# Kernel tuning notes

Hardware: AMD Instinct MI355X
Metric: run time of the kernel (lower is better)

Reference implementation:

```python
import jax, jax.numpy as jnp
import numpy as np

DIM = 1024
HEADS = 8
SCALE = 64 ** (-0.5)  # module uses dimHead=64 even though per-head c = DIM//HEADS = 128
LN_EPS = 1e-3  # keras LayerNormalization default


def _layernorm(t, g, b):
    mu = jnp.mean(t, axis=-1, keepdims=True)
    var = jnp.mean(jnp.square(t - mu), axis=-1, keepdims=True)
    return (t - mu) * jax.lax.rsqrt(var + LN_EPS) * g + b


def setup_inputs() -> dict:
    key = jax.random.key(0)
    ks = jax.random.split(key, 4)
    B, N, D = 4, 2048, DIM
    x = jax.random.normal(ks[0], (B, N, D), dtype=jnp.float32)
    w3 = jax.random.normal(ks[1], (D, 3 * D), dtype=jnp.float32) * (1.0 / np.sqrt(D))
    w1 = jax.random.normal(ks[2], (D, 4 * D), dtype=jnp.float32) * (1.0 / np.sqrt(D))
    w2 = jax.random.normal(ks[3], (4 * D, D), dtype=jnp.float32) * (1.0 / np.sqrt(4 * D))
    return {
        "x": x,
        "ln_g": jnp.ones((D,), jnp.float32),
        "ln_b": jnp.zeros((D,), jnp.float32),
        "w3": w3,
        "b3": jnp.zeros((3 * D,), jnp.float32),
        "w1": w1,
        "b1": jnp.zeros((4 * D,), jnp.float32),
        "w2": w2,
        "b2": jnp.zeros((D,), jnp.float32),
    }


def reference(x, ln_g, ln_b, w3, b3, w1, b1, w2, b2):
    B, N, D = x.shape
    H = HEADS
    C = D // H  # per-head channel dim

    # --- attention branch ---
    y = _layernorm(x, ln_g, ln_b)
    qkv = jax.nn.relu(y @ w3 + b3)  # [B, N, 3D] (note: relu on QKV, as in source)
    # einops 'b n (c h i) -> i b h n c' with i=3: last axis factors as (C, H, 3)
    qkv = qkv.reshape(B, N, C, H, 3)
    qkv = jnp.transpose(qkv, (4, 0, 3, 1, 2))  # [3, B, H, N, C]
    q, k, v = qkv[0], qkv[1], qkv[2]
    scores = jnp.einsum("bhqc,bhkc->bhqk", q, k) * SCALE
    attn = jax.nn.softmax(scores, axis=-1)
    o = jnp.einsum("bhqk,bhkc->bhqc", attn, v)  # [B, H, N, C]
    # 'b h n c -> b n (h c)'
    o = jnp.transpose(o, (0, 2, 1, 3)).reshape(B, N, H * C)
    y = o + x

    # --- MLP branch (shared layernorm params; dropout is identity at inference) ---
    y1 = _layernorm(y, ln_g, ln_b)
    mlp = jax.nn.relu(y1 @ w1 + b1) @ w2 + b2
    return mlp + y
```

## Files before the change

### kernel.cpp

```cpp
#include <hip/hip_runtime.h>
#include <hip/hip_bf16.h>
#include <cstdint>

typedef __attribute__((ext_vector_type(8))) __bf16 bf16x8;
typedef __attribute__((ext_vector_type(4))) float f32x4;
typedef unsigned short u16;

#define DEV static __device__ __forceinline__

constexpr float ATT_SCALE = 0.125f;
constexpr float LN_EPS = 1e-3f;

DEV void gload16(const void* g, void* l) {
  __builtin_amdgcn_global_load_lds((__attribute__((address_space(1))) void*)(g),
                                   (__attribute__((address_space(3))) void*)(l),
                                   16, 0, 0);
}

DEV u16 f2b(float f) { __hip_bfloat16 h = __float2bfloat16(f); return __builtin_bit_cast(u16, h); }

template<int PERM>
__global__ __launch_bounds__(256)
void k_transpose(const float* __restrict__ in, __hip_bfloat16* __restrict__ out,
                 int R, int C) {
  __shared__ float t[64][65];
  int d0 = blockIdx.x * 64, k0 = blockIdx.y * 64;
  int tid = threadIdx.x;
  int c64 = tid & 63, r4 = tid >> 6;
#pragma unroll
  for (int i = 0; i < 16; i++) {
    int kr = i * 4 + r4;
    t[c64][kr] = in[(size_t)(k0 + kr) * C + d0 + c64];
  }
  __syncthreads();
#pragma unroll
  for (int i = 0; i < 16; i++) {
    int dr = i * 4 + r4;
    int d = d0 + dr;
    int jp = PERM ? ((d % 3) * 1024 + ((d / 3) & 7) * 128 + (d / 24)) : d;
    out[(size_t)jp * R + k0 + c64] = __float2bfloat16(t[dr][c64]);
  }
}

__global__ __launch_bounds__(256)
void k_ln(const float* __restrict__ in, const float* __restrict__ g,
          const float* __restrict__ b, __hip_bfloat16* __restrict__ out) {
  int row = blockIdx.x, tid = threadIdx.x;
  const float4* in4 = (const float4*)(in + (size_t)row * 1024);
  float4 v = in4[tid];
  float s = v.x + v.y + v.z + v.w;
  float ss = v.x * v.x + v.y * v.y + v.z * v.z + v.w * v.w;
#pragma unroll
  for (int off = 32; off; off >>= 1) { s += __shfl_down(s, off); ss += __shfl_down(ss, off); }
  __shared__ float red[8];
  int w = tid >> 6, lane = tid & 63;
  if (lane == 0) { red[w] = s; red[4 + w] = ss; }
  __syncthreads();
  if (tid == 0) {
    float S = red[0] + red[1] + red[2] + red[3];
    float SS = red[4] + red[5] + red[6] + red[7];
    float mu = S * (1.f / 1024.f);
    float var = SS * (1.f / 1024.f) - mu * mu;
    red[0] = mu; red[1] = rsqrtf(var + LN_EPS);
  }
  __syncthreads();
  float mu = red[0], rs = red[1];
  int c = tid * 4;
  ushort4 o;
  o.x = f2b((v.x - mu) * rs * g[c + 0] + b[c + 0]);
  o.y = f2b((v.y - mu) * rs * g[c + 1] + b[c + 1]);
  o.z = f2b((v.z - mu) * rs * g[c + 2] + b[c + 2]);
  o.w = f2b((v.w - mu) * rs * g[c + 3] + b[c + 3]);
  ((ushort4*)((u16*)out + (size_t)row * 1024))[tid] = o;
}

template<int MODE>
__global__ __launch_bounds__(256, 2)
void k_gemm(const __hip_bfloat16* __restrict__ A,
            const __hip_bfloat16* __restrict__ Bt,
            const float* __restrict__ bias,
            const float* __restrict__ resid,
            float* __restrict__ outF,
            __hip_bfloat16* __restrict__ outQ,
            __hip_bfloat16* __restrict__ outK,
            __hip_bfloat16* __restrict__ outV,
            int K, int Nout) {
  __shared__ alignas(16) __hip_bfloat16 Asm[128 * 32];
  __shared__ alignas(16) __hip_bfloat16 Bsm[128 * 32];
  int tid = threadIdx.x, w = tid >> 6, lane = tid & 63;
  int wr = w >> 1, wc = w & 1;
  int lr = lane >> 4, lc = lane & 15;
  int m0 = blockIdx.y * 128, n0 = blockIdx.x * 128;
  f32x4 acc[4][4] = {};
  const __hip_bfloat16* aG = A + (size_t)(m0 + (tid >> 2)) * K + (tid & 3) * 8;
  const __hip_bfloat16* bG = Bt + (size_t)(n0 + (tid >> 2)) * K + (tid & 3) * 8;
  char* aB = (char*)Asm + w * 1024;
  char* bB = (char*)Bsm + w * 1024;
  for (int k0 = 0; k0 < K; k0 += 32) {
    gload16(aG + k0, aB);
    gload16(aG + (size_t)64 * K + k0, aB + 4096);
    gload16(bG + k0, bB);
    gload16(bG + (size_t)64 * K + k0, bB + 4096);
    __syncthreads();
    bf16x8 af[4], bfr[4];
#pragma unroll
    for (int mi = 0; mi < 4; mi++)
      af[mi] = *(const bf16x8*)(Asm + (wr * 64 + mi * 16 + lc) * 32 + lr * 8);
#pragma unroll
    for (int ni = 0; ni < 4; ni++)
      bfr[ni] = *(const bf16x8*)(Bsm + (wc * 64 + ni * 16 + lc) * 32 + lr * 8);
#pragma unroll
    for (int mi = 0; mi < 4; mi++)
#pragma unroll
      for (int ni = 0; ni < 4; ni++)
        acc[mi][ni] = __builtin_amdgcn_mfma_f32_16x16x32_bf16(af[mi], bfr[ni], acc[mi][ni], 0, 0, 0);
    __syncthreads();
  }
#pragma unroll
  for (int mi = 0; mi < 4; mi++) {
#pragma unroll
    for (int ni = 0; ni < 4; ni++) {
      int jp = n0 + wc * 64 + ni * 16 + lc;
#pragma unroll
      for (int r = 0; r < 4; r++) {
        int m = m0 + wr * 64 + mi * 16 + lr * 4 + r;
        float v = acc[mi][ni][r];
        if (MODE == 0) {
          int i = jp >> 10, h = (jp >> 7) & 7, c = jp & 127;
          v += bias[c * 24 + h * 3 + i];
          v = fmaxf(v, 0.f);
          __hip_bfloat16 bv = __float2bfloat16(v);
          int b_ = m >> 11, n = m & 2047;
          size_t bh = (size_t)(b_ * 8 + h);
          if (i == 0)      outQ[(bh * 2048 + n) * 128 + c] = bv;
          else if (i == 1) outK[(bh * 2048 + n) * 128 + c] = bv;
          else             outV[(bh * 128 + c) * 2048 + n] = bv;
        } else if (MODE == 1) {
          v += bias[jp];
          v = fmaxf(v, 0.f);
          outQ[(size_t)m * Nout + jp] = __float2bfloat16(v);
        } else {
          v += bias[jp] + resid[(size_t)m * Nout + jp];
          outF[(size_t)m * Nout + jp] = v;
        }
      }
    }
  }
}

__global__ __launch_bounds__(256, 3)
void k_attn(const __hip_bfloat16* __restrict__ qb,
            const __hip_bfloat16* __restrict__ kb,
            const __hip_bfloat16* __restrict__ vtb,
            const float* __restrict__ x,
            float* __restrict__ y) {
  __shared__ alignas(16) __hip_bfloat16 Kl[64 * 128];
  __shared__ alignas(16) __hip_bfloat16 Vl[128 * 64];
  __shared__ alignas(16) __hip_bfloat16 Pl[4 * 16 * 72];
  int tid = threadIdx.x, w = tid >> 6, lane = tid & 63;
  int lr = lane >> 4, lc = lane & 15;
  int sxz = (lc & 7) << 3;
  int qt = blockIdx.x, bh = blockIdx.y;
  int b_ = bh >> 3, h = bh & 7;
  int q0 = qt * 64;
  size_t bhN = (size_t)bh * 2048;

  bf16x8 qf[4];
#pragma unroll
  for (int ks = 0; ks < 4; ks++)
    qf[ks] = *(const bf16x8*)(qb + (bhN + q0 + w * 16 + lc) * 128 + ks * 32 + lr * 8);

  f32x4 oacc[8] = {};
  float mrun[4], lrun[4];
#pragma unroll
  for (int r = 0; r < 4; r++) { mrun[r] = -1e30f; lrun[r] = 0.f; }

  int krow = tid >> 4;
  int kcol = ((tid & 15) * 8) ^ ((krow & 7) << 3);
  const __hip_bfloat16* kG = kb + (bhN + krow) * 128 + kcol;
  int vrow = tid >> 3;
  int vcol = ((tid & 7) * 8) ^ ((vrow & 7) << 3);
  const __hip_bfloat16* vG = vtb + ((size_t)bh * 128 + vrow) * 2048 + vcol;
  char* kB = (char*)Kl + w * 1024;
  char* vB = (char*)Vl + w * 1024;

  for (int kv0 = 0; kv0 < 2048; kv0 += 64) {
#pragma unroll
    for (int p = 0; p < 4; p++)
      gload16(kG + (size_t)(kv0 + p * 16) * 128, kB + p * 4096);
#pragma unroll
    for (int p = 0; p < 4; p++)
      gload16(vG + kv0 + (size_t)p * 32 * 2048, vB + p * 4096);
    __syncthreads();

    f32x4 sf[4] = {};
#pragma unroll
    for (int ks = 0; ks < 4; ks++) {
      bf16x8 kfr[4];
#pragma unroll
      for (int ni = 0; ni < 4; ni++)
        kfr[ni] = *(const bf16x8*)(Kl + (ni * 16 + lc) * 128 + ((ks * 32 + lr * 8) ^ sxz));
#pragma unroll
      for (int ni = 0; ni < 4; ni++)
        sf[ni] = __builtin_amdgcn_mfma_f32_16x16x32_bf16(qf[ks], kfr[ni], sf[ni], 0, 0, 0);
    }

#pragma unroll
    for (int r = 0; r < 4; r++) {
      float tmax = fmaxf(fmaxf(sf[0][r], sf[1][r]), fmaxf(sf[2][r], sf[3][r]));
#pragma unroll
      for (int off = 1; off < 16; off <<= 1) tmax = fmaxf(tmax, __shfl_xor(tmax, off, 16));
      tmax *= ATT_SCALE;
      float mnew = fmaxf(mrun[r], tmax);
      float alpha = __expf(mrun[r] - mnew);
      mrun[r] = mnew;
      float rs = 0.f;
#pragma unroll
      for (int ni = 0; ni < 4; ni++) {
        float p = __expf(sf[ni][r] * ATT_SCALE - mnew);
        sf[ni][r] = p;
        rs += p;
      }
#pragma unroll
      for (int off = 1; off < 16; off <<= 1) rs += __shfl_xor(rs, off, 16);
      lrun[r] = lrun[r] * alpha + rs;
#pragma unroll
      for (int nc = 0; nc < 8; nc++) oacc[nc][r] *= alpha;
    }

#pragma unroll
    for (int ni = 0; ni < 4; ni++)
#pragma unroll
      for (int r = 0; r < 4; r++)
        Pl[w * 1152 + (lr * 4 + r) * 72 + ni * 16 + lc] = __float2bfloat16(sf[ni][r]);
    asm volatile("s_waitcnt lgkmcnt(0)" ::: "memory");

#pragma unroll
    for (int ks2 = 0; ks2 < 2; ks2++) {
      bf16x8 pa = *(const bf16x8*)(Pl + w * 1152 + lc * 72 + ks2 * 32 + lr * 8);
#pragma unroll
      for (int nc = 0; nc < 8; nc++) {
        bf16x8 vf = *(const bf16x8*)(Vl + (nc * 16 + lc) * 64 + ((ks2 * 32 + lr * 8) ^ sxz));
        oacc[nc] = __builtin_amdgcn_mfma_f32_16x16x32_bf16(pa, vf, oacc[nc], 0, 0, 0);
      }
    }
    __syncthreads();
  }

#pragma unroll
  for (int r = 0; r < 4; r++) {
    int n = q0 + w * 16 + lr * 4 + r;
    float inv = 1.f / lrun[r];
    size_t base = ((size_t)(b_ * 2048 + n)) * 1024 + h * 128;
#pragma unroll
    for (int nc = 0; nc < 8; nc++) {
      int c = nc * 16 + lc;
      y[base + c] = oacc[nc][r] * inv + x[base + c];
    }
  }
}

extern "C" void kernel_launch(void* const* d_in, const int* in_sizes, int n_in,
                              void* d_out, int out_size, void* d_ws, size_t ws_size,
                              hipStream_t stream) {
  const float* x   = (const float*)d_in[0];
  const float* lng = (const float*)d_in[1];
  const float* lnb = (const float*)d_in[2];
  const float* w3  = (const float*)d_in[3];
  const float* b3  = (const float*)d_in[4];
  const float* w1  = (const float*)d_in[5];
  const float* b1  = (const float*)d_in[6];
  const float* w2  = (const float*)d_in[7];
  const float* b2  = (const float*)d_in[8];
  float* out = (float*)d_out;

  constexpr size_t M = 8192;
  __hip_bfloat16* w3t  = (__hip_bfloat16*)d_ws;
  __hip_bfloat16* w1t  = w3t + (size_t)3072 * 1024;
  __hip_bfloat16* w2t  = w1t + (size_t)4096 * 1024;
  __hip_bfloat16* xln  = w2t + (size_t)4096 * 1024;
  __hip_bfloat16* qb   = xln + M * 1024;
  __hip_bfloat16* kbuf = qb + M * 1024;
  __hip_bfloat16* vtb  = kbuf + M * 1024;
  __hip_bfloat16* hmid = qb;

  k_transpose<1><<<dim3(48, 16), 256, 0, stream>>>(w3, w3t, 1024, 3072);
  k_transpose<0><<<dim3(64, 16), 256, 0, stream>>>(w1, w1t, 1024, 4096);
  k_transpose<0><<<dim3(16, 64), 256, 0, stream>>>(w2, w2t, 4096, 1024);
  k_ln<<<dim3(M), 256, 0, stream>>>(x, lng, lnb, xln);
  k_gemm<0><<<dim3(24, 64), 256, 0, stream>>>(xln, w3t, b3, nullptr, nullptr,
                                              qb, kbuf, vtb, 1024, 3072);
  k_attn<<<dim3(32, 32), 256, 0, stream>>>(qb, kbuf, vtb, x, out);
  k_ln<<<dim3(M), 256, 0, stream>>>(out, lng, lnb, xln);
  k_gemm<1><<<dim3(32, 64), 256, 0, stream>>>(xln, w1t, b1, nullptr, nullptr,
                                              hmid, nullptr, nullptr, 1024, 4096);
  k_gemm<2><<<dim3(8, 64), 256, 0, stream>>>(hmid, w2t, b2, out, out,
                                             nullptr, nullptr, nullptr, 4096, 1024);
}
```

Baseline: 569.4 us.

## Add triple-buffered 256-row GEMM for QKV/FC1 and double-buffer attention K/V

```diff
diff --git a/kernel.cpp b/kernel.cpp
--- a/kernel.cpp
+++ b/kernel.cpp
@@ -74,16 +74,118 @@
   ((ushort4*)((u16*)out + (size_t)row * 1024))[tid] = o;
 }
 
-template<int MODE>
+template<int NI, int MODE>
+__global__ __launch_bounds__(512, NI == 2 ? 4 : 2)
+void k_gemm2(const __hip_bfloat16* __restrict__ A,
+             const __hip_bfloat16* __restrict__ Bt,
+             const float* __restrict__ bias,
+             __hip_bfloat16* __restrict__ outQ,
+             __hip_bfloat16* __restrict__ outK,
+             __hip_bfloat16* __restrict__ outV,
+             int K, int Nout) {
+  constexpr int BN = NI * 64;
+  constexpr int ASZ = 256 * 32;
+  constexpr int BSZ = BN * 32;
+  constexpr int SLOT = ASZ + BSZ;
+  __shared__ alignas(16) __hip_bfloat16 lds[3 * SLOT];
+  int tid = threadIdx.x, wid = tid >> 6, lane = tid & 63;
+  int wr = wid >> 2, wc = wid & 3, lr = lane >> 4, lc = lane & 15;
+  int nwg = gridDim.x;
+  int wg = ((int)blockIdx.x & 7) * (nwg >> 3) + ((int)blockIdx.x >> 3);
+  int mtile = wg & 31, ntile = wg >> 5;
+  int m0 = mtile * 256, n0 = ntile * BN;
+  int NT = K >> 5;
+
+  int sw = ((tid >> 3) & 3) << 3;
+  const __hip_bfloat16* aS = A + (size_t)(m0 + (tid >> 2)) * K + (((tid & 3) * 8) ^ sw);
+  const __hip_bfloat16* bS = Bt + (size_t)(n0 + (tid >> 2)) * K + (((tid & 3) * 8) ^ sw);
+  const size_t K128 = (size_t)128 * K;
+
+  f32x4 acc[8][NI] = {};
+
+  auto STAGE = [&](int t, int slot) {
+    char* s = (char*)(lds + slot * SLOT);
+    const __hip_bfloat16* ap = aS + t * 32;
+    gload16(ap, s + tid * 16);
+    gload16(ap + K128, s + tid * 16 + 8192);
+    const __hip_bfloat16* bp = bS + t * 32;
+    gload16(bp, s + tid * 16 + 16384);
+    if constexpr (NI == 4) gload16(bp + K128, s + tid * 16 + 24576);
+  };
+
+  STAGE(0, 0); STAGE(1, 1);
+  if constexpr (NI == 2) asm volatile("s_waitcnt vmcnt(3)" ::: "memory");
+  else                   asm volatile("s_waitcnt vmcnt(4)" ::: "memory");
+  __builtin_amdgcn_s_barrier();
+  asm volatile("" ::: "memory");
+
+  int axor = ((lc >> 1) & 3) << 3;
+  int s_cur = 0;
+  for (int t = 0; t < NT; ++t) {
+    if (t + 2 < NT) { int s2 = s_cur + 2; if (s2 >= 3) s2 -= 3; STAGE(t + 2, s2); }
+    const __hip_bfloat16* As = lds + s_cur * SLOT;
+    const __hip_bfloat16* Bs = As + ASZ;
+    bf16x8 af[8], bfr[NI];
+#pragma unroll
+    for (int mi = 0; mi < 8; mi++)
+      af[mi] = *(const bf16x8*)(As + (wr * 128 + mi * 16 + lc) * 32 + ((lr * 8) ^ axor));
+#pragma unroll
+    for (int ni = 0; ni < NI; ni++)
+      bfr[ni] = *(const bf16x8*)(Bs + (wc * (BN / 4) + ni * 16 + lc) * 32 + ((lr * 8) ^ axor));
+    __builtin_amdgcn_s_setprio(1);
+#pragma unroll
+    for (int mi = 0; mi < 8; mi++)
+#pragma unroll
+      for (int ni = 0; ni < NI; ni++)
+        acc[mi][ni] = __builtin_amdgcn_mfma_f32_16x16x32_bf16(af[mi], bfr[ni], acc[mi][ni], 0, 0, 0);
+    __builtin_amdgcn_s_setprio(0);
+    if (t + 2 < NT) {
+      if constexpr (NI == 2) asm volatile("s_waitcnt vmcnt(3)" ::: "memory");
+      else                   asm volatile("s_waitcnt vmcnt(4)" ::: "memory");
+    } else {
+      asm volatile("s_waitcnt vmcnt(0)" ::: "memory");
+    }
+    asm volatile("" ::: "memory");
+    __builtin_amdgcn_s_barrier();
+    asm volatile("" ::: "memory");
+    s_cur = s_cur + 1; if (s_cur >= 3) s_cur = 0;
+  }
+
+#pragma unroll
+  for (int mi = 0; mi < 8; mi++) {
+#pragma unroll
+    for (int ni = 0; ni < NI; ni++) {
+      int jp = n0 + wc * (BN / 4) + ni * 16 + lc;
+#pragma unroll
+      for (int r = 0; r < 4; r++) {
+        int m = m0 + wr * 128 + mi * 16 + lr * 4 + r;
+        float v = acc[mi][ni][r];
+        if (MODE == 0) {
+          int i = jp >> 10, h = (jp >> 7) & 7, c = jp & 127;
+          v += bias[c * 24 + h * 3 + i];
+          v = fmaxf(v, 0.f);
+          __hip_bfloat16 bv = __float2bfloat16(v);
+          int b_ = m >> 11, n = m & 2047;
+          size_t bh = (size_t)(b_ * 8 + h);
+          if (i == 0)      outQ[(bh * 2048 + n) * 128 + c] = bv;
+          else if (i == 1) outK[(bh * 2048 + n) * 128 + c] = bv;
+          else             outV[(bh * 128 + c) * 2048 + n] = bv;
+        } else {
+          v += bias[jp];
+          v = fmaxf(v, 0.f);
+          outQ[(size_t)m * Nout + jp] = __float2bfloat16(v);
+        }
+      }
+    }
+  }
+}
+
 __global__ __launch_bounds__(256, 2)
 void k_gemm(const __hip_bfloat16* __restrict__ A,
             const __hip_bfloat16* __restrict__ Bt,
             const float* __restrict__ bias,
             const float* __restrict__ resid,
             float* __restrict__ outF,
-            __hip_bfloat16* __restrict__ outQ,
-            __hip_bfloat16* __restrict__ outK,
-            __hip_bfloat16* __restrict__ outV,
             int K, int Nout) {
   __shared__ alignas(16) __hip_bfloat16 Asm[128 * 32];
   __shared__ alignas(16) __hip_bfloat16 Bsm[128 * 32];
@@ -124,38 +226,21 @@
 #pragma unroll
       for (int r = 0; r < 4; r++) {
         int m = m0 + wr * 64 + mi * 16 + lr * 4 + r;
-        float v = acc[mi][ni][r];
-        if (MODE == 0) {
-          int i = jp >> 10, h = (jp >> 7) & 7, c = jp & 127;
-          v += bias[c * 24 + h * 3 + i];
-          v = fmaxf(v, 0.f);
-          __hip_bfloat16 bv = __float2bfloat16(v);
-          int b_ = m >> 11, n = m & 2047;
-          size_t bh = (size_t)(b_ * 8 + h);
-          if (i == 0)      outQ[(bh * 2048 + n) * 128 + c] = bv;
-          else if (i == 1) outK[(bh * 2048 + n) * 128 + c] = bv;
-          else             outV[(bh * 128 + c) * 2048 + n] = bv;
-        } else if (MODE == 1) {
-          v += bias[jp];
-          v = fmaxf(v, 0.f);
-          outQ[(size_t)m * Nout + jp] = __float2bfloat16(v);
-        } else {
-          v += bias[jp] + resid[(size_t)m * Nout + jp];
-          outF[(size_t)m * Nout + jp] = v;
-        }
+        float v = acc[mi][ni][r] + bias[jp] + resid[(size_t)m * Nout + jp];
+        outF[(size_t)m * Nout + jp] = v;
       }
     }
   }
 }
 
-__global__ __launch_bounds__(256, 3)
+__global__ __launch_bounds__(256, 2)
 void k_attn(const __hip_bfloat16* __restrict__ qb,
             const __hip_bfloat16* __restrict__ kb,
             const __hip_bfloat16* __restrict__ vtb,
             const float* __restrict__ x,
             float* __restrict__ y) {
-  __shared__ alignas(16) __hip_bfloat16 Kl[64 * 128];
-  __shared__ alignas(16) __hip_bfloat16 Vl[128 * 64];
+  __shared__ alignas(16) __hip_bfloat16 Kl[2][64 * 128];
+  __shared__ alignas(16) __hip_bfloat16 Vl[2][128 * 64];
   __shared__ alignas(16) __hip_bfloat16 Pl[4 * 16 * 72];
   int tid = threadIdx.x, w = tid >> 6, lane = tid & 63;
   int lr = lane >> 4, lc = lane & 15;
@@ -181,29 +266,40 @@
   int vrow = tid >> 3;
   int vcol = ((tid & 7) * 8) ^ ((vrow & 7) << 3);
   const __hip_bfloat16* vG = vtb + ((size_t)bh * 128 + vrow) * 2048 + vcol;
-  char* kB = (char*)Kl + w * 1024;
-  char* vB = (char*)Vl + w * 1024;
-
-  for (int kv0 = 0; kv0 < 2048; kv0 += 64) {
+
+  auto STAGEKV = [&](int kv0, int buf) {
+    char* kB = (char*)(&Kl[buf][0]) + w * 1024;
+    char* vB = (char*)(&Vl[buf][0]) + w * 1024;
 #pragma unroll
     for (int p = 0; p < 4; p++)
       gload16(kG + (size_t)(kv0 + p * 16) * 128, kB + p * 4096);
 #pragma unroll
     for (int p = 0; p < 4; p++)
       gload16(vG + kv0 + (size_t)p * 32 * 2048, vB + p * 4096);
-    __syncthreads();
+  };
+
+  STAGEKV(0, 0);
+  __syncthreads();
+
+  for (int it = 0; it < 32; ++it) {
+    int buf = it & 1;
+    if (it < 31) STAGEKV((it + 1) * 64, buf ^ 1);
+    const __hip_bfloat16* Kb = &Kl[buf][0];
+    const __hip_bfloat16* Vb = &Vl[buf][0];
 
     f32x4 sf[4] = {};
+    __builtin_amdgcn_s_setprio(1);
 #pragma unroll
     for (int ks = 0; ks < 4; ks++) {
       bf16x8 kfr[4];
 #pragma unroll
       for (int ni = 0; ni < 4; ni++)
-        kfr[ni] = *(const bf16x8*)(Kl + (ni * 16 + lc) * 128 + ((ks * 32 + lr * 8) ^ sxz));
+        kfr[ni] = *(const bf16x8*)(Kb + (ni * 16 + lc) * 128 + ((ks * 32 + lr * 8) ^ sxz));
 #pragma unroll
       for (int ni = 0; ni < 4; ni++)
         sf[ni] = __builtin_amdgcn_mfma_f32_16x16x32_bf16(qf[ks], kfr[ni], sf[ni], 0, 0, 0);
     }
+    __builtin_amdgcn_s_setprio(0);
 
 #pragma unroll
     for (int r = 0; r < 4; r++) {
@@ -235,15 +331,17 @@
         Pl[w * 1152 + (lr * 4 + r) * 72 + ni * 16 + lc] = __float2bfloat16(sf[ni][r]);
     asm volatile("s_waitcnt lgkmcnt(0)" ::: "memory");
 
+    __builtin_amdgcn_s_setprio(1);
 #pragma unroll
     for (int ks2 = 0; ks2 < 2; ks2++) {
       bf16x8 pa = *(const bf16x8*)(Pl + w * 1152 + lc * 72 + ks2 * 32 + lr * 8);
 #pragma unroll
       for (int nc = 0; nc < 8; nc++) {
-        bf16x8 vf = *(const bf16x8*)(Vl + (nc * 16 + lc) * 64 + ((ks2 * 32 + lr * 8) ^ sxz));
+        bf16x8 vf = *(const bf16x8*)(Vb + (nc * 16 + lc) * 64 + ((ks2 * 32 + lr * 8) ^ sxz));
         oacc[nc] = __builtin_amdgcn_mfma_f32_16x16x32_bf16(pa, vf, oacc[nc], 0, 0, 0);
       }
     }
+    __builtin_amdgcn_s_setprio(0);
     __syncthreads();
   }
 
@@ -288,12 +386,9 @@
   k_transpose<0><<<dim3(64, 16), 256, 0, stream>>>(w1, w1t, 1024, 4096);
   k_transpose<0><<<dim3(16, 64), 256, 0, stream>>>(w2, w2t, 4096, 1024);
   k_ln<<<dim3(M), 256, 0, stream>>>(x, lng, lnb, xln);
-  k_gemm<0><<<dim3(24, 64), 256, 0, stream>>>(xln, w3t, b3, nullptr, nullptr,
-                                              qb, kbuf, vtb, 1024, 3072);
+  k_gemm2<2, 0><<<dim3(768), 512, 0, stream>>>(xln, w3t, b3, qb, kbuf, vtb, 1024, 3072);
   k_attn<<<dim3(32, 32), 256, 0, stream>>>(qb, kbuf, vtb, x, out);
   k_ln<<<dim3(M), 256, 0, stream>>>(out, lng, lnb, xln);
-  k_gemm<1><<<dim3(32, 64), 256, 0, stream>>>(xln, w1t, b1, nullptr, nullptr,
-                                              hmid, nullptr, nullptr, 1024, 4096);
-  k_gemm<2><<<dim3(8, 64), 256, 0, stream>>>(hmid, w2t, b2, out, out,
-                                             nullptr, nullptr, nullptr, 4096, 1024);
-}
+  k_gemm2<4, 1><<<dim3(512), 512, 0, stream>>>(xln, w1t, b1, hmid, nullptr, nullptr, 1024, 4096);
+  k_gemm<<<dim3(8, 64), 256, 0, stream>>>(hmid, w2t, b2, out, out, 4096, 1024);
+}
```

Measured after the change: 603.3 us. +6.0%, slower.

## Double-buffer K tiles in attention with 512-thread blocks and lazy rescale

Applied to the files above, without the earlier changes.

```diff
diff --git a/kernel.cpp b/kernel.cpp
--- a/kernel.cpp
+++ b/kernel.cpp
@@ -148,21 +148,21 @@
   }
 }
 
-__global__ __launch_bounds__(256, 3)
+__global__ __launch_bounds__(512, 4)
 void k_attn(const __hip_bfloat16* __restrict__ qb,
             const __hip_bfloat16* __restrict__ kb,
             const __hip_bfloat16* __restrict__ vtb,
             const float* __restrict__ x,
             float* __restrict__ y) {
-  __shared__ alignas(16) __hip_bfloat16 Kl[64 * 128];
+  __shared__ alignas(16) __hip_bfloat16 Kl[2][64 * 128];
   __shared__ alignas(16) __hip_bfloat16 Vl[128 * 64];
-  __shared__ alignas(16) __hip_bfloat16 Pl[4 * 16 * 72];
+  __shared__ alignas(16) __hip_bfloat16 Pl[8 * 16 * 72];
   int tid = threadIdx.x, w = tid >> 6, lane = tid & 63;
   int lr = lane >> 4, lc = lane & 15;
   int sxz = (lc & 7) << 3;
   int qt = blockIdx.x, bh = blockIdx.y;
   int b_ = bh >> 3, h = bh & 7;
-  int q0 = qt * 64;
+  int q0 = qt * 128;
   size_t bhN = (size_t)bh * 2048;
 
   bf16x8 qf[4];
@@ -181,51 +181,79 @@
   int vrow = tid >> 3;
   int vcol = ((tid & 7) * 8) ^ ((vrow & 7) << 3);
   const __hip_bfloat16* vG = vtb + ((size_t)bh * 128 + vrow) * 2048 + vcol;
-  char* kB = (char*)Kl + w * 1024;
-  char* vB = (char*)Vl + w * 1024;
-
-  for (int kv0 = 0; kv0 < 2048; kv0 += 64) {
-#pragma unroll
-    for (int p = 0; p < 4; p++)
-      gload16(kG + (size_t)(kv0 + p * 16) * 128, kB + p * 4096);
-#pragma unroll
-    for (int p = 0; p < 4; p++)
-      gload16(vG + kv0 + (size_t)p * 32 * 2048, vB + p * 4096);
-    __syncthreads();
+
+  auto STAGE_K = [&](int kv0, int buf) {
+    char* kB = (char*)(&Kl[buf][0]) + w * 1024;
+#pragma unroll
+    for (int p = 0; p < 2; p++)
+      gload16(kG + (size_t)(kv0 + p * 32) * 128, kB + p * 8192);
+  };
+  auto STAGE_V = [&](int kv0) {
+    char* vB = (char*)(&Vl[0]) + w * 1024;
+#pragma unroll
+    for (int p = 0; p < 2; p++)
+      gload16(vG + kv0 + (size_t)p * 64 * 2048, vB + p * 8192);
+  };
+
+  STAGE_V(0);
+  STAGE_K(0, 0);
+  asm volatile("s_waitcnt vmcnt(0)" ::: "memory");
+  __syncthreads();
+
+  for (int it = 0; it < 32; ++it) {
+    int buf = it & 1;
+    if (it > 0) STAGE_V(it * 64);
+    if (it < 31) STAGE_K((it + 1) * 64, buf ^ 1);
+    const __hip_bfloat16* Kb = &Kl[buf][0];
 
     f32x4 sf[4] = {};
+    __builtin_amdgcn_s_setprio(1);
 #pragma unroll
     for (int ks = 0; ks < 4; ks++) {
       bf16x8 kfr[4];
 #pragma unroll
       for (int ni = 0; ni < 4; ni++)
-        kfr[ni] = *(const bf16x8*)(Kl + (ni * 16 + lc) * 128 + ((ks * 32 + lr * 8) ^ sxz));
+        kfr[ni] = *(const bf16x8*)(Kb + (ni * 16 + lc) * 128 + ((ks * 32 + lr * 8) ^ sxz));
 #pragma unroll
       for (int ni = 0; ni < 4; ni++)
         sf[ni] = __builtin_amdgcn_mfma_f32_16x16x32_bf16(qf[ks], kfr[ni], sf[ni], 0, 0, 0);
     }
-
+    __builtin_amdgcn_s_setprio(0);
+
+    float tmax[4];
+    bool need = false;
 #pragma unroll
     for (int r = 0; r < 4; r++) {
-      float tmax = fmaxf(fmaxf(sf[0][r], sf[1][r]), fmaxf(sf[2][r], sf[3][r]));
-#pragma unroll
-      for (int off = 1; off < 16; off <<= 1) tmax = fmaxf(tmax, __shfl_xor(tmax, off, 16));
-      tmax *= ATT_SCALE;
-      float mnew = fmaxf(mrun[r], tmax);
-      float alpha = __expf(mrun[r] - mnew);
-      mrun[r] = mnew;
+      float tm = fmaxf(fmaxf(sf[0][r], sf[1][r]), fmaxf(sf[2][r], sf[3][r]));
+#pragma unroll
+      for (int off = 1; off < 16; off <<= 1) tm = fmaxf(tm, __shfl_xor(tm, off, 16));
+      tm *= ATT_SCALE;
+      tmax[r] = tm;
+      need = need || (tm > mrun[r] + 8.f);
+    }
+    if (__any(need)) {
+#pragma unroll
+      for (int r = 0; r < 4; r++) {
+        float mnew = fmaxf(mrun[r], tmax[r]);
+        float alpha = __expf(mrun[r] - mnew);
+        mrun[r] = mnew;
+        lrun[r] *= alpha;
+#pragma unroll
+        for (int nc = 0; nc < 8; nc++) oacc[nc][r] *= alpha;
+      }
+    }
+#pragma unroll
+    for (int r = 0; r < 4; r++) {
       float rs = 0.f;
 #pragma unroll
       for (int ni = 0; ni < 4; ni++) {
-        float p = __expf(sf[ni][r] * ATT_SCALE - mnew);
+        float p = __expf(sf[ni][r] * ATT_SCALE - mrun[r]);
         sf[ni][r] = p;
         rs += p;
       }
 #pragma unroll
       for (int off = 1; off < 16; off <<= 1) rs += __shfl_xor(rs, off, 16);
-      lrun[r] = lrun[r] * alpha + rs;
-#pragma unroll
-      for (int nc = 0; nc < 8; nc++) oacc[nc][r] *= alpha;
+      lrun[r] += rs;
     }
 
 #pragma unroll
@@ -233,8 +261,12 @@
 #pragma unroll
       for (int r = 0; r < 4; r++)
         Pl[w * 1152 + (lr * 4 + r) * 72 + ni * 16 + lc] = __float2bfloat16(sf[ni][r]);
-    asm volatile("s_waitcnt lgkmcnt(0)" ::: "memory");
-
+
+    if (it < 31) asm volatile("s_waitcnt vmcnt(2) lgkmcnt(0)" ::: "memory");
+    else         asm volatile("s_waitcnt vmcnt(0) lgkmcnt(0)" ::: "memory");
+    __builtin_amdgcn_s_barrier();
+
+    __builtin_amdgcn_s_setprio(1);
 #pragma unroll
     for (int ks2 = 0; ks2 < 2; ks2++) {
       bf16x8 pa = *(const bf16x8*)(Pl + w * 1152 + lc * 72 + ks2 * 32 + lr * 8);
@@ -244,6 +276,7 @@
         oacc[nc] = __builtin_amdgcn_mfma_f32_16x16x32_bf16(pa, vf, oacc[nc], 0, 0, 0);
       }
     }
+    __builtin_amdgcn_s_setprio(0);
     __syncthreads();
   }
 
@@ -290,7 +323,7 @@
   k_ln<<<dim3(M), 256, 0, stream>>>(x, lng, lnb, xln);
   k_gemm<0><<<dim3(24, 64), 256, 0, stream>>>(xln, w3t, b3, nullptr, nullptr,
                                               qb, kbuf, vtb, 1024, 3072);
-  k_attn<<<dim3(32, 32), 256, 0, stream>>>(qb, kbuf, vtb, x, out);
+  k_attn<<<dim3(16, 32), 512, 0, stream>>>(qb, kbuf, vtb, x, out);
   k_ln<<<dim3(M), 256, 0, stream>>>(out, lng, lnb, xln);
   k_gemm<1><<<dim3(32, 64), 256, 0, stream>>>(xln, w1t, b1, nullptr, nullptr,
                                               hmid, nullptr, nullptr, 1024, 4096);
```

Result: faster. 540.1 us (-5.2%).
